# Kernel tuning notes

Hardware: AMD Instinct MI355X
Metric: run time of the kernel (lower is better)

## Reference

```python
import jax, jax.numpy as jnp
import numpy as np

N = 20000          # num nodes
E = 400000         # num edges
F_NODE = 16        # node_features
F_EDGE = 16        # edge_features
H = 128            # hidden_size
D = 16             # node_embedding_dim
DE = 16            # edge_embedding_dim


def setup_inputs() -> dict:
    key = jax.random.key(0)
    ks = jax.random.split(key, 16)
    s = 0.1
    inp = {
        "x": jax.random.normal(ks[0], (N, F_NODE), jnp.float32),
        "edge_index": jax.random.randint(ks[1], (2, E), 0, N, dtype=jnp.int64),
        "edge_attr": jax.random.normal(ks[2], (E, F_EDGE), jnp.float32),
        # node_embedding: Linear(F_NODE, D)
        "Wn": jax.random.normal(ks[3], (F_NODE, D), jnp.float32) * s,
        "bn": jnp.zeros((D,), jnp.float32),
        # edge_embedding: Linear(F_EDGE, DE)
        "We": jax.random.normal(ks[4], (F_EDGE, DE), jnp.float32) * s,
        "be": jnp.zeros((DE,), jnp.float32),
        # shared edge MLP: Linear(F_EDGE, H) -> ReLU -> Linear(H, 2*D*D)
        "W1": jax.random.normal(ks[5], (F_EDGE, H), jnp.float32) * s,
        "b1": jnp.zeros((H,), jnp.float32),
        "W2": jax.random.normal(ks[6], (H, 2 * D * D), jnp.float32) * s,
        "b2": jnp.zeros((2 * D * D,), jnp.float32),
        # per-layer root weights and biases
        "root1": jax.random.normal(ks[7], (D, D), jnp.float32) * s,
        "bias1": jnp.zeros((D,), jnp.float32),
        "root2": jax.random.normal(ks[8], (D, D), jnp.float32) * s,
        "bias2": jnp.zeros((D,), jnp.float32),
    }
    return inp


def _graph_conv(h, src, dst, edge_attr, W1, b1, W2, b2, root, bias):
    # per-edge weight from shared MLP: [E, 2D*D] -> [E, 2D, D]
    w = jnp.maximum(edge_attr @ W1 + b1, 0.0) @ W2 + b2
    w = w.reshape(E, 2 * D, D)
    # gather endpoint features; x_i = target, x_j = source (PyG flow)
    nf = jnp.concatenate([h[dst], h[src]], axis=1)           # [E, 2D]
    msg = jnp.einsum("ek,ekd->ed", nf, w)                    # [E, D]
    aggr = jax.ops.segment_sum(msg, dst, num_segments=N)     # [N, D]
    return aggr + h @ root + bias


def reference(x, edge_index, edge_attr, Wn, bn, We, be, W1, b1, W2, b2,
              root1, bias1, root2, bias2):
    src, dst = edge_index[0], edge_index[1]
    h = jnp.maximum(x @ Wn + bn, 0.0)                        # node embedding [N, D]
    h = _graph_conv(h, src, dst, edge_attr, W1, b1, W2, b2, root1, bias1)
    h = _graph_conv(h, src, dst, edge_attr, W1, b1, W2, b2, root2, bias2)
    ee = jnp.maximum(edge_attr @ We + be, 0.0)               # edge embedding [E, DE]
    return h, edge_index, ee, jax.nn.log_softmax(ee, axis=-1)
```

## Files before the change

kernel.cpp:

```cpp
#include <hip/hip_runtime.h>
#include <hip/hip_bf16.h>


#define NN 20000
#define NE 400000

typedef unsigned short u16;
typedef unsigned int   u32;
typedef __attribute__((ext_vector_type(8))) short short8;
typedef __attribute__((ext_vector_type(4))) float f32x4;

__device__ __forceinline__ float bf2f(u16 h) {
  union { u32 u; float f; } v; v.u = ((u32)h) << 16; return v.f;
}
__device__ __forceinline__ u16 f2bf(float f) {
  union { float f; u32 u; } v; v.f = f;
  return (u16)((v.u + 0x7FFFu + ((v.u >> 16) & 1u)) >> 16);
}
__device__ __forceinline__ float ldf(const void* p, size_t i, int f32m) {
  return f32m ? ((const float*)p)[i] : bf2f(((const u16*)p)[i]);
}
__device__ __forceinline__ int ldi(const void* p, size_t i, int i64m) {
  return i64m ? (int)((const long long*)p)[i] : ((const int*)p)[i];
}
__device__ __forceinline__ void stf(void* p, size_t i, float v, int f32m) {
  if (f32m) ((float*)p)[i] = v; else ((u16*)p)[i] = f2bf(v);
}

__global__ void k_detect(const u16* __restrict__ x16,
                         const int* __restrict__ ei32, int* __restrict__ flags) {
  int t = blockIdx.x * 256 + threadIdx.x;
  int found_f32 = 0, found_hi = 0;
  for (int i = t; i < NN * 16; i += 64 * 256) {
    u16 v = x16[i];
    if ((v & 0x7F80u) == 0x7F80u) found_f32 = 1;
  }
  for (int i = t; i < 200000; i += 64 * 256)
    if (ei32[2 * i + 1] != 0) found_hi = 1;
  if (__any(found_f32) && (threadIdx.x & 63) == 0) atomicOr(&flags[0], 1);
  if (__any(found_hi) && (threadIdx.x & 63) == 0) atomicOr(&flags[1], 1);
}

__global__ void k_pack_w2(const void* __restrict__ W2, u16* __restrict__ w2p,
                          const int* __restrict__ flags) {
  const int f32m = flags[0];
  int t = blockIdx.x * 256 + threadIdx.x;
  if (t >= 32 * 4 * 64) return;
  int lane = t & 63;
  int ks = (t >> 6) & 3;
  int kb = t >> 8;
  int n = lane & 15, q = lane >> 4;
  for (int j = 0; j < 8; ++j) {
    int h = ks * 32 + q * 8 + j;
    w2p[(size_t)t * 8 + j] = f2bf(ldf(W2, (size_t)h * 512 + kb * 16 + n, f32m));
  }
}

__global__ void k_pack_w1(const void* __restrict__ W1, u16* __restrict__ w1p,
                          const int* __restrict__ flags) {
  const int f32m = flags[0];
  int t = blockIdx.x * 256 + threadIdx.x;
  if (t >= 8 * 64) return;
  int lane = t & 63;
  int n = t >> 6;
  int col = n * 16 + (lane & 15), q = lane >> 4;
  for (int j = 0; j < 8; ++j) {
    int kk = q * 8 + j;
    w1p[(size_t)t * 8 + j] = (kk < 16) ? f2bf(ldf(W1, (size_t)kk * 128 + col, f32m)) : (u16)0;
  }
}

__global__ void k_pack_qd(const void* __restrict__ W2, u16* __restrict__ w2q,
                          u16* __restrict__ w2d, const int* __restrict__ flags) {
  const int f32m = flags[0];
  int t = blockIdx.x * 256 + threadIdx.x;
  if (t >= 8192) return;
  int lane = t & 63, q = lane >> 4, l16 = lane & 15;
  if (t < 4096) {
    int kc = t >> 6;
#pragma unroll
    for (int jj = 0; jj < 8; ++jj) {
      int kj = kc * 32 + q * 8 + jj;
      int j = kj >> 4, ks = kj & 15;
      w2q[(size_t)t * 8 + jj] =
          f2bf(ldf(W2, (size_t)j * 512 + (16 + ks) * 16 + l16, f32m));
    }
  } else {
    int u = t - 4096;
    int ct = u >> 8;
    int jc = (u >> 6) & 3;
#pragma unroll
    for (int jj = 0; jj < 8; ++jj) {
      int j = jc * 32 + q * 8 + jj;
      w2d[(size_t)u * 8 + jj] =
          f2bf(ldf(W2, (size_t)j * 512 + ct * 16 + l16, f32m));
    }
  }
}

__global__ void k_embed(const void* __restrict__ x, const void* __restrict__ Wn,
                        const void* __restrict__ bn, float* __restrict__ h0,
                        const int* __restrict__ flags) {
  const int f32m = flags[0];
  int t = blockIdx.x * 256 + threadIdx.x;
  if (t >= NN * 16) return;
  int n = t >> 4, d = t & 15;
  float acc = ldf(bn, d, f32m);
  for (int k = 0; k < 16; ++k)
    acc += ldf(x, n * 16 + k, f32m) * ldf(Wn, k * 16 + d, f32m);
  h0[t] = fmaxf(acc, 0.f);
}

__global__ void k_count(const void* __restrict__ ei, int* __restrict__ cnt,
                        const int* __restrict__ flags) {
  const int i64m = !flags[1];
  int i = blockIdx.x * 256 + threadIdx.x;
  if (i < NE) atomicAdd(&cnt[ldi(ei, NE + i, i64m)], 1);
}

__global__ void k_scan(const int* __restrict__ cnt, int* __restrict__ rowptr,
                       int* __restrict__ cursor) {
  __shared__ int part[1024];
  int t = threadIdx.x;
  int base = t * 20;
  int s = 0;
  for (int j = 0; j < 20; ++j) { int idx = base + j; if (idx < NN) s += cnt[idx]; }
  part[t] = s;
  __syncthreads();
  for (int off = 1; off < 1024; off <<= 1) {
    int v = (t >= off) ? part[t - off] : 0;
    __syncthreads();
    part[t] += v;
    __syncthreads();
  }
  int run = t ? part[t - 1] : 0;
  for (int j = 0; j < 20; ++j) {
    int idx = base + j;
    if (idx < NN) {
      int c = cnt[idx];
      rowptr[idx] = run; cursor[idx] = run; run += c;
    }
  }
  if (t == 1023) rowptr[NN] = part[1023];
}

__global__ void k_scanp(const int* __restrict__ deg, int* __restrict__ prow,
                        int* __restrict__ cursor) {
  __shared__ int part[1024];
  int t = threadIdx.x;
  int base = t * 20;
  int s = 0;
  for (int j = 0; j < 20; ++j) {
    int idx = base + j;
    if (idx < NN) s += (deg[idx] + 31) & ~31;
  }
  part[t] = s;
  __syncthreads();
  for (int off = 1; off < 1024; off <<= 1) {
    int v = (t >= off) ? part[t - off] : 0;
    __syncthreads();
    part[t] += v;
    __syncthreads();
  }
  int run = t ? part[t - 1] : 0;
  for (int j = 0; j < 20; ++j) {
    int idx = base + j;
    if (idx < NN) {
      int p = (deg[idx] + 31) & ~31;
      prow[idx] = run; cursor[idx] = run; run += p;
    }
  }
  if (t == 1023) prow[NN] = part[1023];
}

__global__ void k_scatter(const void* __restrict__ ei, int* __restrict__ cursor,
                          int* __restrict__ inv, int* __restrict__ srcp,
                          const void* __restrict__ ea, u16* __restrict__ eap,
                          const int* __restrict__ flags) {
  const int f32m = flags[0], i64m = !flags[1];
  int i = blockIdx.x * 256 + threadIdx.x;
  if (i >= NE) return;
  int d = ldi(ei, NE + i, i64m);
  int pos = atomicAdd(&cursor[d], 1);
  if (inv)   inv[i] = pos;
  if (srcp)  srcp[pos] = ldi(ei, i, i64m);
  if (eap) {
    union { uint4 q[2]; u16 h[16]; } o;
    if (f32m) {
      const float4* ep = (const float4*)((const float*)ea + (size_t)i * 16);
      float4 a = ep[0], b = ep[1], c = ep[2], e4 = ep[3];
      o.h[0]=f2bf(a.x);  o.h[1]=f2bf(a.y);  o.h[2]=f2bf(a.z);  o.h[3]=f2bf(a.w);
      o.h[4]=f2bf(b.x);  o.h[5]=f2bf(b.y);  o.h[6]=f2bf(b.z);  o.h[7]=f2bf(b.w);
      o.h[8]=f2bf(c.x);  o.h[9]=f2bf(c.y);  o.h[10]=f2bf(c.z); o.h[11]=f2bf(c.w);
      o.h[12]=f2bf(e4.x); o.h[13]=f2bf(e4.y); o.h[14]=f2bf(e4.z); o.h[15]=f2bf(e4.w);
    } else {
      const uint4* ep = (const uint4*)((const u16*)ea + (size_t)i * 16);
      o.q[0] = ep[0]; o.q[1] = ep[1];
    }
    uint4* dp = (uint4*)(eap + (size_t)pos * 16);
    dp[0] = o.q[0]; dp[1] = o.q[1];
  }
}

__launch_bounds__(256)
__attribute__((amdgpu_waves_per_eu(2, 4)))
__global__ void k_node(const int* __restrict__ prow,
                       const int* __restrict__ deg,
                       const int* __restrict__ srcperm,
                       const u16* __restrict__ eap,
                       const float* __restrict__ hin,
                       const u16* __restrict__ w1p,
                       const void* __restrict__ b1,
                       const u16* __restrict__ w2q,
                       const u16* __restrict__ w2d,
                       const void* __restrict__ b2,
                       const void* __restrict__ root,
                       const void* __restrict__ bias,
                       float* __restrict__ hout, void* __restrict__ out,
                       const int* __restrict__ flags) {
  __shared__ u16   T_lds[4 * 2048];
  __shared__ u32   S_lds[4 * 64];
  __shared__ float hs_lds[4 * 16];
  __shared__ float h_lds[4 * 16];
  __shared__ float part_lds[4 * 256];
  __shared__ float b1_lds[128];
  __shared__ u16   w1_lds[4096];
  __shared__ u32   BB_lds[4][320];
  const int f32m = flags[0];
  const int t = threadIdx.x;
  const int lane = t & 63, w = t >> 6;
  const int q = lane >> 4, l16 = lane & 15;
  const int n0 = blockIdx.x * 4;
  const short8 z8 = {0,0,0,0,0,0,0,0};

  if (t < 64) h_lds[t] = hin[(size_t)(n0 + (t >> 4)) * 16 + (t & 15)];
  if (t < 128) b1_lds[t] = ldf(b1, t, f32m);
  {
    const uint4* src = (const uint4*)w1p;
    uint4* dst = (uint4*)w1_lds;
    dst[t] = src[t];
    dst[t + 256] = src[t + 256];
  }

  short8 ONES;
  { union { u32 u[4]; short8 s; } o;
    o.u[0] = 0x3F803F80u; o.u[1] = 0x3F803F80u;
    o.u[2] = 0x3F803F80u; o.u[3] = 0x3F803F80u; ONES = o.s; }

  __syncthreads();

  const int nb = w;
  {
    const int n  = n0 + nb;
    const int beg = prow[n];
    const int end = beg + deg[n];

    f32x4 accT[8];
    float S8[8];
    f32x4 accH = {0.f, 0.f, 0.f, 0.f};
#pragma unroll
    for (int c = 0; c < 8; ++c) {
      accT[c][0] = 0.f; accT[c][1] = 0.f; accT[c][2] = 0.f; accT[c][3] = 0.f;
      S8[c] = 0.f;
    }

    for (int g = beg; g < end; g += 32) {
      int src_l = (lane < 32) ? srcperm[g + lane] : 0;
      union { u32 u[4]; short8 s; } Ahi, Alo, Amk;
#pragma unroll
      for (int jp = 0; jp < 4; ++jp) {
        const int k0 = q * 8 + 2 * jp, k1 = k0 + 1;
        int s0 = __shfl(src_l, k0);
        int s1 = __shfl(src_l, k1);
        float h0 = hin[(size_t)s0 * 16 + l16];
        float h1 = hin[(size_t)s1 * 16 + l16];
        const int v0 = (g + k0 < end);
        const int v1 = (g + k1 < end);
        h0 = v0 ? h0 : 0.f;
        h1 = v1 ? h1 : 0.f;
        union { float f; u32 u; } b0, b1u; b0.f = h0; b1u.f = h1;
        u32 hi0 = b0.u >> 16, hi1 = b1u.u >> 16;
        union { u32 u; float f; } r0, r1; r0.u = hi0 << 16; r1.u = hi1 << 16;
        u32 lo0 = f2bf(h0 - r0.f), lo1 = f2bf(h1 - r1.f);
        Ahi.u[jp] = hi0 | (hi1 << 16);
        Alo.u[jp] = lo0 | (lo1 << 16);
        Amk.u[jp] = (v0 ? 0x3F80u : 0u) | (v1 ? 0x3F800000u : 0u);
      }

      short8 ea0 = z8, ea1 = z8;
      if (q < 2) {
        ea0 = *(const short8*)(eap + (size_t)(g + l16) * 16 + q * 8);
        ea1 = *(const short8*)(eap + (size_t)(g + 16 + l16) * 16 + q * 8);
      }

#pragma unroll
      for (int c = 0; c < 8; ++c) {
        short8 Wf = *(const short8*)&w1_lds[c * 512 + lane * 8];
        f32x4 ca = {0.f, 0.f, 0.f, 0.f}, cb = {0.f, 0.f, 0.f, 0.f};
        ca = __builtin_amdgcn_mfma_f32_16x16x32_bf16(ea0, Wf, ca, 0, 0, 0);
        cb = __builtin_amdgcn_mfma_f32_16x16x32_bf16(ea1, Wf, cb, 0, 0, 0);
        float bb = b1_lds[c * 16 + l16];
        u32 p00 = (u32)f2bf(fmaxf(ca[0] + bb, 0.f)) |
                  ((u32)f2bf(fmaxf(ca[1] + bb, 0.f)) << 16);
        u32 p01 = (u32)f2bf(fmaxf(ca[2] + bb, 0.f)) |
                  ((u32)f2bf(fmaxf(ca[3] + bb, 0.f)) << 16);
        u32 p10 = (u32)f2bf(fmaxf(cb[0] + bb, 0.f)) |
                  ((u32)f2bf(fmaxf(cb[1] + bb, 0.f)) << 16);
        u32 p11 = (u32)f2bf(fmaxf(cb[2] + bb, 0.f)) |
                  ((u32)f2bf(fmaxf(cb[3] + bb, 0.f)) << 16);
        u32* bw = &BB_lds[w][l16 * 20];
        uint2 w0; w0.x = p00; w0.y = p01;
        uint2 w1v; w1v.x = p10; w1v.y = p11;
        *(uint2*)&bw[q * 2]     = w0;
        *(uint2*)&bw[8 + q * 2] = w1v;
        short8 Bf = *(const short8*)&bw[q * 4];
        accT[c] = __builtin_amdgcn_mfma_f32_16x16x32_bf16(Ahi.s, Bf, accT[c], 0, 0, 0);
        accT[c] = __builtin_amdgcn_mfma_f32_16x16x32_bf16(Alo.s, Bf, accT[c], 0, 0, 0);
        f32x4 cs = {0.f, 0.f, 0.f, 0.f};
        cs = __builtin_amdgcn_mfma_f32_16x16x32_bf16(Amk.s, Bf, cs, 0, 0, 0);
        S8[c] += cs[0];
      }
      accH = __builtin_amdgcn_mfma_f32_16x16x32_bf16(Ahi.s, ONES, accH, 0, 0, 0);
      accH = __builtin_amdgcn_mfma_f32_16x16x32_bf16(Alo.s, ONES, accH, 0, 0, 0);
    }

    {
      char* Tl = (char*)T_lds;
#pragma unroll
      for (int c = 0; c < 8; ++c) {
        u32 p0 = (u32)f2bf(accT[c][0]) | ((u32)f2bf(accT[c][1]) << 16);
        u32 p1 = (u32)f2bf(accT[c][2]) | ((u32)f2bf(accT[c][3]) << 16);
        int b   = (c * 16 + l16) * 32 + q * 8;
        int key = ((nb ^ (c * 8 + (l16 >> 1))) & 7) << 4;
        uint2 pv; pv.x = p0; pv.y = p1;
        *(uint2*)(Tl + (size_t)nb * 4096 + (b ^ key)) = pv;
      }
      if (q == 0) {
        u16* s16 = (u16*)S_lds;
#pragma unroll
        for (int c = 0; c < 8; ++c)
          s16[nb * 128 + c * 16 + l16] = f2bf(S8[c]);
      }
      if (l16 == 0) *(f32x4*)&hs_lds[nb * 16 + q * 4] = accH;
    }
  }
  __syncthreads();

  const int row = l16;
  f32x4 c1 = {0.f, 0.f, 0.f, 0.f};
  {
    const short8* w2qf = (const short8*)w2q;
#pragma unroll
    for (int kk = 0; kk < 16; ++kk) {
      int kc = w * 16 + kk;
      int off = ((row & 3) * 4096 + kc * 64 + q * 16) ^ ((((row ^ kc) & 7)) << 4);
      short8 af = *(const short8*)((const char*)T_lds + off);
      if (row >= 4) af = z8;
      short8 bf = w2qf[kc * 64 + lane];
      c1 = __builtin_amdgcn_mfma_f32_16x16x32_bf16(af, bf, c1, 0, 0, 0);
    }
  }
  f32x4 c2_0 = {0,0,0,0}, c2_1 = {0,0,0,0}, c2_2 = {0,0,0,0}, c2_3 = {0,0,0,0};
  {
    short8 as0, as1, as2, as3;
    {
      const u32* sb = S_lds + (row & 3) * 64 + q * 4;
      as0 = *(const short8*)(sb + 0);
      as1 = *(const short8*)(sb + 16);
      as2 = *(const short8*)(sb + 32);
      as3 = *(const short8*)(sb + 48);
      if (row >= 4) { as0 = z8; as1 = z8; as2 = z8; as3 = z8; }
    }
    const short8* w2df = (const short8*)w2d;
#pragma unroll
    for (int ci = 0; ci < 4; ++ci) {
      int ct = w * 4 + ci;
      f32x4 cc = {0.f, 0.f, 0.f, 0.f};
      cc = __builtin_amdgcn_mfma_f32_16x16x32_bf16(as0, w2df[(ct * 4 + 0) * 64 + lane], cc, 0, 0, 0);
      cc = __builtin_amdgcn_mfma_f32_16x16x32_bf16(as1, w2df[(ct * 4 + 1) * 64 + lane], cc, 0, 0, 0);
      cc = __builtin_amdgcn_mfma_f32_16x16x32_bf16(as2, w2df[(ct * 4 + 2) * 64 + lane], cc, 0, 0, 0);
      cc = __builtin_amdgcn_mfma_f32_16x16x32_bf16(as3, w2df[(ct * 4 + 3) * 64 + lane], cc, 0, 0, 0);
      if (ci == 0) c2_0 = cc; else if (ci == 1) c2_1 = cc;
      else if (ci == 2) c2_2 = cc; else c2_3 = cc;
    }
  }
#pragma unroll
  for (int r = 0; r < 4; ++r) {
    int nrow = q * 4 + r;
    const float* hp = h_lds + (nrow & 3) * 16 + w * 4;
    float a = c1[r];
    a += hp[0] * c2_0[r];
    a += hp[1] * c2_1[r];
    a += hp[2] * c2_2[r];
    a += hp[3] * c2_3[r];
    part_lds[w * 256 + nrow * 16 + l16] = a;
  }
  __syncthreads();

  if (t < 64) {
    int nb2 = t >> 4, d = t & 15;
    int n = n0 + nb2;
    float acc = part_lds[nb2 * 16 + d] + part_lds[256 + nb2 * 16 + d] +
                part_lds[512 + nb2 * 16 + d] + part_lds[768 + nb2 * 16 + d];
    float dg = (float)deg[n];
    acc += ldf(bias, d, f32m);
#pragma unroll
    for (int k = 0; k < 16; ++k) {
      float hv = h_lds[nb2 * 16 + k];
      acc += hv * (ldf(root, (size_t)k * 16 + d, f32m) +
                   dg * ldf(b2, (size_t)k * 16 + d, f32m));
      acc += hs_lds[nb2 * 16 + k] * ldf(b2, (size_t)256 + k * 16 + d, f32m);
    }
    if (hout) hout[(size_t)n * 16 + d] = acc;
    else      stf(out, (size_t)n * 16 + d, acc, f32m);
  }
}

__launch_bounds__(256, 2)
__global__ void k_edge(const void* __restrict__ ea, const void* __restrict__ ei,
                       const float* __restrict__ hprev,
                       const u16* __restrict__ w2p, const u16* __restrict__ w1p,
                       const void* __restrict__ b1, const void* __restrict__ b2,
                       u16* __restrict__ msg16, float* __restrict__ aggr,
                       const int* __restrict__ inv,
                       const int* __restrict__ flags, int use_csr) {
  __shared__ u16   a2_lds[128 * 136];
  __shared__ float nfT[32 * 132];
  __shared__ float msg_lds[128 * 17];
  __shared__ float b1_lds[128];
  __shared__ int   dst_lds[128];

  const int f32m = flags[0], i64m = !flags[1];
  const int t = threadIdx.x;
  const int lane = t & 63, w = t >> 6;
  const int q = lane >> 4, l16 = lane & 15;
  const int e0 = blockIdx.x * 128;

  short8 B[8][4];
  {
    const short8* w2pf = (const short8*)w2p;
#pragma unroll
    for (int i = 0; i < 8; ++i)
#pragma unroll
      for (int ks = 0; ks < 4; ++ks)
        B[i][ks] = w2pf[((w * 8 + i) * 4 + ks) * 64 + lane];
  }
  float b2v[8];
#pragma unroll
  for (int i = 0; i < 8; ++i) b2v[i] = ldf(b2, (w * 8 + i) * 16 + l16, f32m);
  short8 W1f[8];
  {
    const short8* w1pf = (const short8*)w1p;
#pragma unroll
    for (int n = 0; n < 8; ++n) W1f[n] = w1pf[n * 64 + lane];
  }
  if (t < 128) b1_lds[t] = ldf(b1, t, f32m);

  {
    int e = t >> 1, hh = t & 1;
    int node = hh ? ldi(ei, e0 + e, i64m) : ldi(ei, NE + e0 + e, i64m);
    const float4* hp = (const float4*)(hprev + (size_t)node * 16);
    float4 h0v = hp[0], h1v = hp[1], h2v = hp[2], h3v = hp[3];
    float* col = nfT + (size_t)(hh * 16) * 132 + e;
    col[0 * 132] = h0v.x; col[1 * 132] = h0v.y; col[2 * 132] = h0v.z; col[3 * 132] = h0v.w;
    col[4 * 132] = h1v.x; col[5 * 132] = h1v.y; col[6 * 132] = h1v.z; col[7 * 132] = h1v.w;
    col[8 * 132] = h2v.x; col[9 * 132] = h2v.y; col[10 * 132] = h2v.z; col[11 * 132] = h2v.w;
    col[12 * 132] = h3v.x; col[13 * 132] = h3v.y; col[14 * 132] = h3v.z; col[15 * 132] = h3v.w;
    if (!hh) {
      if (use_csr) dst_lds[e] = inv[e0 + e];
      else         dst_lds[e] = node;
    }
    float* mz = msg_lds + e * 17 + hh * 8;
#pragma unroll
    for (int k2 = 0; k2 < 8; ++k2) mz[k2] = 0.f;
  }
  __syncthreads();

#pragma unroll
  for (int mm = 0; mm < 2; ++mm) {
    int m = w * 2 + mm;
    union { short8 s; u16 h[8]; } ua;
    if (q < 2) {
      if (f32m) {
        const float* er = (const float*)ea + ((size_t)(e0 + m * 16 + l16) * 16 + q * 8);
        float4 f0 = *(const float4*)er;
        float4 f1 = *(const float4*)(er + 4);
        ua.h[0] = f2bf(f0.x); ua.h[1] = f2bf(f0.y); ua.h[2] = f2bf(f0.z); ua.h[3] = f2bf(f0.w);
        ua.h[4] = f2bf(f1.x); ua.h[5] = f2bf(f1.y); ua.h[6] = f2bf(f1.z); ua.h[7] = f2bf(f1.w);
      } else {
        ua.s = *(const short8*)((const u16*)ea + ((size_t)(e0 + m * 16 + l16) * 16 + q * 8));
      }
    } else {
#pragma unroll
      for (int j = 0; j < 8; ++j) ua.h[j] = 0;
    }
    short8 A = ua.s;
#pragma unroll
    for (int n = 0; n < 8; ++n) {
      f32x4 c = {0.f, 0.f, 0.f, 0.f};
      c = __builtin_amdgcn_mfma_f32_16x16x32_bf16(A, W1f[n], c, 0, 0, 0);
      float bb = b1_lds[n * 16 + l16];
#pragma unroll
      for (int r = 0; r < 4; ++r)
        a2_lds[(m * 16 + q * 4 + r) * 136 + n * 16 + l16] =
            f2bf(fmaxf(c[r] + bb, 0.f));
    }
  }
  __syncthreads();

#pragma unroll 1
  for (int mi = 0; mi < 8; ++mi) {
    int m = (mi + w * 2) & 7;
    const short8* ap = (const short8*)&a2_lds[(m * 16 + l16) * 136 + q * 8];
    short8 A0 = ap[0], A1 = ap[4], A2f = ap[8], A3 = ap[12];
    float mr0 = 0.f, mr1 = 0.f, mr2 = 0.f, mr3 = 0.f;
#pragma unroll
    for (int i = 0; i < 8; ++i) {
      f32x4 c = {b2v[i], b2v[i], b2v[i], b2v[i]};
      c = __builtin_amdgcn_mfma_f32_16x16x32_bf16(A0, B[i][0], c, 0, 0, 0);
      c = __builtin_amdgcn_mfma_f32_16x16x32_bf16(A1, B[i][1], c, 0, 0, 0);
      c = __builtin_amdgcn_mfma_f32_16x16x32_bf16(A2f, B[i][2], c, 0, 0, 0);
      c = __builtin_amdgcn_mfma_f32_16x16x32_bf16(A3, B[i][3], c, 0, 0, 0);
      int kb = w * 8 + i;
      f32x4 nf4 = *(const f32x4*)&nfT[(size_t)kb * 132 + m * 16 + q * 4];
      mr0 += nf4[0] * c[0];
      mr1 += nf4[1] * c[1];
      mr2 += nf4[2] * c[2];
      mr3 += nf4[3] * c[3];
    }
    int eb = (m * 16 + q * 4) * 17 + l16;
    atomicAdd(&msg_lds[eb + 0 * 17], mr0);
    atomicAdd(&msg_lds[eb + 1 * 17], mr1);
    atomicAdd(&msg_lds[eb + 2 * 17], mr2);
    atomicAdd(&msg_lds[eb + 3 * 17], mr3);
  }
  __syncthreads();

  {
    int e = t >> 1, dh = t & 1;
    const float* mp = msg_lds + e * 17 + dh * 8;
    if (use_csr) {
      int pos = dst_lds[e];
      union { uint4 qv; u16 h[8]; } pk;
#pragma unroll
      for (int dd = 0; dd < 8; ++dd) pk.h[dd] = f2bf(mp[dd]);
      *(uint4*)(msg16 + (size_t)pos * 16 + dh * 8) = pk.qv;
    } else {
      int dnode = dst_lds[e];
      float* ap2 = aggr + (size_t)dnode * 16 + dh * 8;
#pragma unroll
      for (int dd = 0; dd < 8; ++dd) atomicAdd(ap2 + dd, mp[dd]);
    }
  }
}

__global__ void k_gather(const u16* __restrict__ msg16,
                         const int* __restrict__ rowptr,
                         const float* __restrict__ h_old,
                         const void* __restrict__ root,
                         const void* __restrict__ bias,
                         float* __restrict__ h_new, void* __restrict__ out,
                         const int* __restrict__ flags) {
  const int f32m = flags[0];
  __shared__ float R[256];
  __shared__ float Bv[16];
  int tt = threadIdx.x;
  R[tt] = ldf(root, tt, f32m);
  if (tt < 16) Bv[tt] = ldf(bias, tt, f32m);
  __syncthreads();
  int t = blockIdx.x * 256 + tt;
  if (t >= NN * 16) return;
  int n = t >> 4, d = t & 15;
  float acc = Bv[d];
#pragma unroll
  for (int k = 0; k < 16; ++k) acc += h_old[n * 16 + k] * R[k * 16 + d];
  int beg = rowptr[n], end = rowptr[n + 1];
  for (int i = beg; i < end; ++i)
    acc += bf2f(msg16[(size_t)i * 16 + d]);
  if (h_new) h_new[t] = acc;
  else       stf(out, t, acc, f32m);
}

__global__ void k_combine(const float* __restrict__ h_old,
                          const float* __restrict__ aggr,
                          const void* __restrict__ root,
                          const void* __restrict__ bias,
                          float* __restrict__ h_new, void* __restrict__ out,
                          const int* __restrict__ flags) {
  const int f32m = flags[0];
  int t = blockIdx.x * 256 + threadIdx.x;
  if (t >= NN * 16) return;
  int n = t >> 4, d = t & 15;
  float acc = aggr[t] + ldf(bias, d, f32m);
  for (int k = 0; k < 16; ++k)
    acc += h_old[n * 16 + k] * ldf(root, (size_t)k * 16 + d, f32m);
  if (h_new) h_new[t] = acc;
  else       stf(out, t, acc, f32m);
}

__global__ void k_ee(const void* __restrict__ ea, const void* __restrict__ We,
                     const void* __restrict__ be, void* __restrict__ out,
                     const int* __restrict__ flags) {
  const int f32m = flags[0];
  __shared__ float W[256];
  __shared__ float Bv[16];
  int t = threadIdx.x;
  W[t] = ldf(We, t, f32m);
  if (t < 16) Bv[t] = ldf(be, t, f32m);
  __syncthreads();
  int e = blockIdx.x * 256 + t;
  if (e >= NE) return;
  float v[16];
  if (f32m) {
    const float4* ep = (const float4*)((const float*)ea + (size_t)e * 16);
    float4 r0 = ep[0], r1 = ep[1], r2 = ep[2], r3 = ep[3];
    v[0]=r0.x; v[1]=r0.y; v[2]=r0.z; v[3]=r0.w;
    v[4]=r1.x; v[5]=r1.y; v[6]=r1.z; v[7]=r1.w;
    v[8]=r2.x; v[9]=r2.y; v[10]=r2.z; v[11]=r2.w;
    v[12]=r3.x; v[13]=r3.y; v[14]=r3.z; v[15]=r3.w;
  } else {
    union { uint4 qv[2]; u16 h[16]; } rw;
    const uint4* ep = (const uint4*)((const u16*)ea + (size_t)e * 16);
    rw.qv[0] = ep[0]; rw.qv[1] = ep[1];
#pragma unroll
    for (int k = 0; k < 16; ++k) v[k] = bf2f(rw.h[k]);
  }
  float o[16];
  float mx = 0.f;
#pragma unroll
  for (int d = 0; d < 16; ++d) {
    float acc = Bv[d];
#pragma unroll
    for (int k = 0; k < 16; ++k) acc += v[k] * W[k * 16 + d];
    acc = fmaxf(acc, 0.f);
    o[d] = acc;
    mx = fmaxf(mx, acc);
  }
  float s = 0.f;
#pragma unroll
  for (int d = 0; d < 16; ++d) s += __expf(o[d] - mx);
  float lse = mx + __logf(s);
  const size_t off_ee = 1120000, off_ls = 7520000;
  if (f32m) {
    union { float4 fv; float f[4]; } pe, pl;
    float* oe = (float*)out + off_ee + (size_t)e * 16;
    float* ol = (float*)out + off_ls + (size_t)e * 16;
#pragma unroll
    for (int g = 0; g < 4; ++g) {
#pragma unroll
      for (int d = 0; d < 4; ++d) { pe.f[d] = o[g*4+d]; pl.f[d] = o[g*4+d] - lse; }
      ((float4*)oe)[g] = pe.fv;
      ((float4*)ol)[g] = pl.fv;
    }
  } else {
    union { uint4 qv[2]; u16 h[16]; } pe, pl;
#pragma unroll
    for (int d = 0; d < 16; ++d) {
      pe.h[d] = f2bf(o[d]);
      pl.h[d] = f2bf(o[d] - lse);
    }
    uint4* oe = (uint4*)((u16*)out + off_ee + (size_t)e * 16);
    uint4* ol = (uint4*)((u16*)out + off_ls + (size_t)e * 16);
    oe[0] = pe.qv[0]; oe[1] = pe.qv[1];
    ol[0] = pl.qv[0]; ol[1] = pl.qv[1];
  }
}

__global__ void k_idx(const void* __restrict__ ei, void* __restrict__ out,
                      const int* __restrict__ flags) {
  const int f32m = flags[0], i64m = !flags[1];
  int i = blockIdx.x * 256 + threadIdx.x;
  if (i >= 2 * NE) return;
  float v = i64m ? (float)((const long long*)ei)[i] : (float)((const int*)ei)[i];
  stf(out, (size_t)320000 + i, v, f32m);
}

extern "C" void kernel_launch(void* const* d_in, const int* in_sizes, int n_in,
                              void* d_out, int out_size, void* d_ws, size_t ws_size,
                              hipStream_t stream) {
  const void* x     = d_in[0];
  const void* ei    = d_in[1];
  const void* ea    = d_in[2];
  const void* Wn    = d_in[3];
  const void* bn    = d_in[4];
  const void* We    = d_in[5];
  const void* be    = d_in[6];
  const void* W1    = d_in[7];
  const void* b1    = d_in[8];
  const void* W2    = d_in[9];
  const void* b2    = d_in[10];
  const void* root1 = d_in[11];
  const void* bias1 = d_in[12];
  const void* root2 = d_in[13];
  const void* bias2 = d_in[14];

  char* ws = (char*)d_ws;
  const size_t need_new = 39659296;

  if (ws_size >= need_new) {
    int*   flags   = (int*)ws;
    float* h0      = (float*)(ws + 16);
    float* h1      = (float*)(ws + 1280016);
    u16*   w1p     = (u16*)(ws + 2560016);
    u16*   w2q     = (u16*)(ws + 2568208);
    u16*   w2d     = (u16*)(ws + 2633744);
    int*   deg     = (int*)(ws + 2699280);
    int*   prow    = (int*)(ws + 2779280);
    int*   cursor  = (int*)(ws + 2859296);
    int*   srcperm = (int*)(ws + 2939296);
    u16*   eap     = (u16*)(ws + 7019296);

    hipMemsetAsync(flags, 0, 16, stream);
    hipMemsetAsync(deg, 0, 80000, stream);
    hipMemsetAsync(srcperm, 0, 36720000, stream);
    k_detect<<<64, 256, 0, stream>>>((const u16*)x, (const int*)ei, flags);
    k_pack_w1<<<2, 256, 0, stream>>>(W1, w1p, flags);
    k_pack_qd<<<32, 256, 0, stream>>>(W2, w2q, w2d, flags);
    k_embed<<<1250, 256, 0, stream>>>(x, Wn, bn, h0, flags);

    k_count<<<1563, 256, 0, stream>>>(ei, deg, flags);
    k_scanp<<<1, 1024, 0, stream>>>(deg, prow, cursor);
    k_scatter<<<1563, 256, 0, stream>>>(ei, cursor, nullptr, srcperm, ea, eap, flags);

    k_node<<<5000, 256, 0, stream>>>(prow, deg, srcperm, eap, h0, w1p, b1, w2q, w2d,
                                     b2, root1, bias1, h1, nullptr, flags);
    k_node<<<5000, 256, 0, stream>>>(prow, deg, srcperm, eap, h1, w1p, b1, w2q, w2d,
                                     b2, root2, bias2, nullptr, d_out, flags);

    k_ee<<<1563, 256, 0, stream>>>(ea, We, be, d_out, flags);
    k_idx<<<3125, 256, 0, stream>>>(ei, d_out, flags);
    return;
  }

  int*   flags  = (int*)ws;
  float* h0     = (float*)(ws + 16);
  float* h1     = (float*)(ws + 1280016);
  u16*   w2p    = (u16*)(ws + 2560016);
  u16*   w1p    = (u16*)(ws + 2691088);
  u16*   msg16  = (u16*)(ws + 2699280);
  int*   rowptr = (int*)(ws + 15499280);
  int*   cursor = (int*)(ws + 15579296);
  int*   inv    = (int*)(ws + 15659296);
  const size_t need_csr = 17259296;
  float* aggr = (float*)(ws + 2699280);
  const int use_csr = (ws_size >= need_csr) ? 1 : 0;

  hipMemsetAsync(flags, 0, 16, stream);
  k_detect<<<64, 256, 0, stream>>>((const u16*)x, (const int*)ei, flags);
  k_pack_w2<<<32, 256, 0, stream>>>(W2, w2p, flags);
  k_pack_w1<<<2, 256, 0, stream>>>(W1, w1p, flags);
  k_embed<<<1250, 256, 0, stream>>>(x, Wn, bn, h0, flags);

  if (use_csr) {
    hipMemsetAsync(cursor, 0, NN * 4, stream);
    k_count<<<1563, 256, 0, stream>>>(ei, cursor, flags);
    k_scan<<<1, 1024, 0, stream>>>(cursor, rowptr, cursor);
    k_scatter<<<1563, 256, 0, stream>>>(ei, cursor, inv, nullptr, nullptr, nullptr, flags);

    k_edge<<<3125, 256, 0, stream>>>(ea, ei, h0, w2p, w1p, b1, b2, msg16, nullptr, inv, flags, 1);
    k_gather<<<1250, 256, 0, stream>>>(msg16, rowptr, h0, root1, bias1, h1, nullptr, flags);
    k_edge<<<3125, 256, 0, stream>>>(ea, ei, h1, w2p, w1p, b1, b2, msg16, nullptr, inv, flags, 1);
    k_gather<<<1250, 256, 0, stream>>>(msg16, rowptr, h1, root2, bias2, nullptr, d_out, flags);
  } else {
    hipMemsetAsync(aggr, 0, (size_t)NN * 16 * 4, stream);
    k_edge<<<3125, 256, 0, stream>>>(ea, ei, h0, w2p, w1p, b1, b2, nullptr, aggr, nullptr, flags, 0);
    k_combine<<<1250, 256, 0, stream>>>(h0, aggr, root1, bias1, h1, nullptr, flags);
    hipMemsetAsync(aggr, 0, (size_t)NN * 16 * 4, stream);
    k_edge<<<3125, 256, 0, stream>>>(ea, ei, h1, w2p, w1p, b1, b2, nullptr, aggr, nullptr, flags, 0);
    k_combine<<<1250, 256, 0, stream>>>(h1, aggr, root2, bias2, nullptr, d_out, flags);
  }

  k_ee<<<1563, 256, 0, stream>>>(ea, We, be, d_out, flags);
  k_idx<<<3125, 256, 0, stream>>>(ei, d_out, flags);
}
```

Measured before the change: 370.0 us.

## Fuse setup kernels into one launch and precompute bf16 hi/lo node features

Merges weight packing, node embedding, degree counting, edge embedding/log-softmax and index output into a single multi-role kernel, cutting several launches and memsets. Node features are also stored as a precomputed bf16 hi/lo pair, so the gather loop in k_node no longer does the split per edge. The MLP bias is folded into the MFMA accumulator init, and k_detect now uses more blocks. This costs extra workspace and an extra store per node feature.

```diff
diff --git a/kernel.cpp b/kernel.cpp
--- a/kernel.cpp
+++ b/kernel.cpp
@@ -17,6 +17,12 @@
   union { float f; u32 u; } v; v.f = f;
   return (u16)((v.u + 0x7FFFu + ((v.u >> 16) & 1u)) >> 16);
 }
+__device__ __forceinline__ u32 splitpk(float h) {
+  union { float f; u32 u; } uu; uu.f = h;
+  u32 hi = uu.u >> 16;
+  union { u32 u; float f; } rr; rr.u = hi << 16;
+  return (hi << 16) | (u32)f2bf(h - rr.f);
+}
 __device__ __forceinline__ float ldf(const void* p, size_t i, int f32m) {
   return f32m ? ((const float*)p)[i] : bf2f(((const u16*)p)[i]);
 }
@@ -30,15 +36,147 @@
 __global__ void k_detect(const u16* __restrict__ x16,
                          const int* __restrict__ ei32, int* __restrict__ flags) {
   int t = blockIdx.x * 256 + threadIdx.x;
+  int stride = gridDim.x * 256;
   int found_f32 = 0, found_hi = 0;
-  for (int i = t; i < NN * 16; i += 64 * 256) {
+  for (int i = t; i < NN * 16; i += stride) {
     u16 v = x16[i];
     if ((v & 0x7F80u) == 0x7F80u) found_f32 = 1;
   }
-  for (int i = t; i < 200000; i += 64 * 256)
+  for (int i = t; i < 200000; i += stride)
     if (ei32[2 * i + 1] != 0) found_hi = 1;
   if (__any(found_f32) && (threadIdx.x & 63) == 0) atomicOr(&flags[0], 1);
   if (__any(found_hi) && (threadIdx.x & 63) == 0) atomicOr(&flags[1], 1);
+}
+
+__global__ void k_misc(const void* __restrict__ W1, u16* __restrict__ w1p,
+                       const void* __restrict__ W2, u16* __restrict__ w2q,
+                       u16* __restrict__ w2d,
+                       const void* __restrict__ x, const void* __restrict__ Wn,
+                       const void* __restrict__ bn, float* __restrict__ h0,
+                       u32* __restrict__ h0s,
+                       const void* __restrict__ ei, int* __restrict__ deg,
+                       const void* __restrict__ ea, const void* __restrict__ We,
+                       const void* __restrict__ be, void* __restrict__ out,
+                       const int* __restrict__ flags) {
+  const int f32m = flags[0], i64m = !flags[1];
+  const int b = blockIdx.x, tid = threadIdx.x;
+  __shared__ float W[256];
+  __shared__ float Bv[16];
+
+  if (b < 2) {
+    int t = b * 256 + tid;
+    int lane = t & 63;
+    int n = t >> 6;
+    int col = n * 16 + (lane & 15), q = lane >> 4;
+    for (int j = 0; j < 8; ++j) {
+      int kk = q * 8 + j;
+      w1p[(size_t)t * 8 + j] = (kk < 16) ? f2bf(ldf(W1, (size_t)kk * 128 + col, f32m)) : (u16)0;
+    }
+  } else if (b < 34) {
+    int t = (b - 2) * 256 + tid;
+    int lane = t & 63, q = lane >> 4, l16 = lane & 15;
+    if (t < 4096) {
+      int kc = t >> 6;
+#pragma unroll
+      for (int jj = 0; jj < 8; ++jj) {
+        int kj = kc * 32 + q * 8 + jj;
+        int j = kj >> 4, ks = kj & 15;
+        w2q[(size_t)t * 8 + jj] =
+            f2bf(ldf(W2, (size_t)j * 512 + (16 + ks) * 16 + l16, f32m));
+      }
+    } else {
+      int u = t - 4096;
+      int ct = u >> 8;
+      int jc = (u >> 6) & 3;
+#pragma unroll
+      for (int jj = 0; jj < 8; ++jj) {
+        int j = jc * 32 + q * 8 + jj;
+        w2d[(size_t)u * 8 + jj] =
+            f2bf(ldf(W2, (size_t)j * 512 + ct * 16 + l16, f32m));
+      }
+    }
+  } else if (b < 1284) {
+    int t = (b - 34) * 256 + tid;
+    if (t < NN * 16) {
+      int n = t >> 4, d = t & 15;
+      float acc = ldf(bn, d, f32m);
+      for (int k = 0; k < 16; ++k)
+        acc += ldf(x, n * 16 + k, f32m) * ldf(Wn, k * 16 + d, f32m);
+      float h = fmaxf(acc, 0.f);
+      h0[t] = h;
+      h0s[t] = splitpk(h);
+    }
+  } else if (b < 2847) {
+    int i = (b - 1284) * 256 + tid;
+    if (i < NE) atomicAdd(&deg[ldi(ei, NE + i, i64m)], 1);
+  } else if (b < 4410) {
+    int t = tid;
+    W[t] = ldf(We, t, f32m);
+    if (t < 16) Bv[t] = ldf(be, t, f32m);
+    __syncthreads();
+    int e = (b - 2847) * 256 + t;
+    if (e >= NE) return;
+    float v[16];
+    if (f32m) {
+      const float4* ep = (const float4*)((const float*)ea + (size_t)e * 16);
+      float4 r0 = ep[0], r1 = ep[1], r2 = ep[2], r3 = ep[3];
+      v[0]=r0.x; v[1]=r0.y; v[2]=r0.z; v[3]=r0.w;
+      v[4]=r1.x; v[5]=r1.y; v[6]=r1.z; v[7]=r1.w;
+      v[8]=r2.x; v[9]=r2.y; v[10]=r2.z; v[11]=r2.w;
+      v[12]=r3.x; v[13]=r3.y; v[14]=r3.z; v[15]=r3.w;
+    } else {
+      union { uint4 qv[2]; u16 h[16]; } rw;
+      const uint4* ep = (const uint4*)((const u16*)ea + (size_t)e * 16);
+      rw.qv[0] = ep[0]; rw.qv[1] = ep[1];
+#pragma unroll
+      for (int k = 0; k < 16; ++k) v[k] = bf2f(rw.h[k]);
+    }
+    float o[16];
+    float mx = 0.f;
+#pragma unroll
+    for (int d = 0; d < 16; ++d) {
+      float acc = Bv[d];
+#pragma unroll
+      for (int k = 0; k < 16; ++k) acc += v[k] * W[k * 16 + d];
+      acc = fmaxf(acc, 0.f);
+      o[d] = acc;
+      mx = fmaxf(mx, acc);
+    }
+    float s = 0.f;
+#pragma unroll
+    for (int d = 0; d < 16; ++d) s += __expf(o[d] - mx);
+    float lse = mx + __logf(s);
+    const size_t off_ee = 1120000, off_ls = 7520000;
+    if (f32m) {
+      union { float4 fv; float f[4]; } pe, pl;
+      float* oe = (float*)out + off_ee + (size_t)e * 16;
+      float* ol = (float*)out + off_ls + (size_t)e * 16;
+#pragma unroll
+      for (int g = 0; g < 4; ++g) {
+#pragma unroll
+        for (int d = 0; d < 4; ++d) { pe.f[d] = o[g*4+d]; pl.f[d] = o[g*4+d] - lse; }
+        ((float4*)oe)[g] = pe.fv;
+        ((float4*)ol)[g] = pl.fv;
+      }
+    } else {
+      union { uint4 qv[2]; u16 h[16]; } pe, pl;
+#pragma unroll
+      for (int d = 0; d < 16; ++d) {
+        pe.h[d] = f2bf(o[d]);
+        pl.h[d] = f2bf(o[d] - lse);
+      }
+      uint4* oe = (uint4*)((u16*)out + off_ee + (size_t)e * 16);
+      uint4* ol = (uint4*)((u16*)out + off_ls + (size_t)e * 16);
+      oe[0] = pe.qv[0]; oe[1] = pe.qv[1];
+      ol[0] = pl.qv[0]; ol[1] = pl.qv[1];
+    }
+  } else {
+    int i = (b - 4410) * 256 + tid;
+    if (i < 2 * NE) {
+      float v = i64m ? (float)((const long long*)ei)[i] : (float)((const int*)ei)[i];
+      stf(out, (size_t)320000 + i, v, f32m);
+    }
+  }
 }
 
 __global__ void k_pack_w2(const void* __restrict__ W2, u16* __restrict__ w2p,
@@ -67,34 +205,6 @@
   for (int j = 0; j < 8; ++j) {
     int kk = q * 8 + j;
     w1p[(size_t)t * 8 + j] = (kk < 16) ? f2bf(ldf(W1, (size_t)kk * 128 + col, f32m)) : (u16)0;
-  }
-}
-
-__global__ void k_pack_qd(const void* __restrict__ W2, u16* __restrict__ w2q,
-                          u16* __restrict__ w2d, const int* __restrict__ flags) {
-  const int f32m = flags[0];
-  int t = blockIdx.x * 256 + threadIdx.x;
-  if (t >= 8192) return;
-  int lane = t & 63, q = lane >> 4, l16 = lane & 15;
-  if (t < 4096) {
-    int kc = t >> 6;
-#pragma unroll
-    for (int jj = 0; jj < 8; ++jj) {
-      int kj = kc * 32 + q * 8 + jj;
-      int j = kj >> 4, ks = kj & 15;
-      w2q[(size_t)t * 8 + jj] =
-          f2bf(ldf(W2, (size_t)j * 512 + (16 + ks) * 16 + l16, f32m));
-    }
-  } else {
-    int u = t - 4096;
-    int ct = u >> 8;
-    int jc = (u >> 6) & 3;
-#pragma unroll
-    for (int jj = 0; jj < 8; ++jj) {
-      int j = jc * 32 + q * 8 + jj;
-      w2d[(size_t)u * 8 + jj] =
-          f2bf(ldf(W2, (size_t)j * 512 + ct * 16 + l16, f32m));
-    }
   }
 }
 
@@ -209,6 +319,7 @@
                        const int* __restrict__ srcperm,
                        const u16* __restrict__ eap,
                        const float* __restrict__ hin,
+                       const u32* __restrict__ hsin,
                        const u16* __restrict__ w1p,
                        const void* __restrict__ b1,
                        const u16* __restrict__ w2q,
@@ -216,7 +327,8 @@
                        const void* __restrict__ b2,
                        const void* __restrict__ root,
                        const void* __restrict__ bias,
-                       float* __restrict__ hout, void* __restrict__ out,
+                       float* __restrict__ hout, u32* __restrict__ hsout,
+                       void* __restrict__ out,
                        const int* __restrict__ flags) {
   __shared__ u16   T_lds[4 * 2048];
   __shared__ u32   S_lds[4 * 64];
@@ -272,18 +384,14 @@
         const int k0 = q * 8 + 2 * jp, k1 = k0 + 1;
         int s0 = __shfl(src_l, k0);
         int s1 = __shfl(src_l, k1);
-        float h0 = hin[(size_t)s0 * 16 + l16];
-        float h1 = hin[(size_t)s1 * 16 + l16];
+        u32 v0d = hsin[(size_t)s0 * 16 + l16];
+        u32 v1d = hsin[(size_t)s1 * 16 + l16];
         const int v0 = (g + k0 < end);
         const int v1 = (g + k1 < end);
-        h0 = v0 ? h0 : 0.f;
-        h1 = v1 ? h1 : 0.f;
-        union { float f; u32 u; } b0, b1u; b0.f = h0; b1u.f = h1;
-        u32 hi0 = b0.u >> 16, hi1 = b1u.u >> 16;
-        union { u32 u; float f; } r0, r1; r0.u = hi0 << 16; r1.u = hi1 << 16;
-        u32 lo0 = f2bf(h0 - r0.f), lo1 = f2bf(h1 - r1.f);
-        Ahi.u[jp] = hi0 | (hi1 << 16);
-        Alo.u[jp] = lo0 | (lo1 << 16);
+        if (!v0) v0d = 0;
+        if (!v1) v1d = 0;
+        Ahi.u[jp] = (v0d >> 16) | (v1d & 0xFFFF0000u);
+        Alo.u[jp] = (v0d & 0xFFFFu) | (v1d << 16);
         Amk.u[jp] = (v0 ? 0x3F80u : 0u) | (v1 ? 0x3F800000u : 0u);
       }
 
@@ -296,18 +404,18 @@
 #pragma unroll
       for (int c = 0; c < 8; ++c) {
         short8 Wf = *(const short8*)&w1_lds[c * 512 + lane * 8];
-        f32x4 ca = {0.f, 0.f, 0.f, 0.f}, cb = {0.f, 0.f, 0.f, 0.f};
+        float bb = b1_lds[c * 16 + l16];
+        f32x4 ca = {bb, bb, bb, bb}, cb = {bb, bb, bb, bb};
         ca = __builtin_amdgcn_mfma_f32_16x16x32_bf16(ea0, Wf, ca, 0, 0, 0);
         cb = __builtin_amdgcn_mfma_f32_16x16x32_bf16(ea1, Wf, cb, 0, 0, 0);
-        float bb = b1_lds[c * 16 + l16];
-        u32 p00 = (u32)f2bf(fmaxf(ca[0] + bb, 0.f)) |
-                  ((u32)f2bf(fmaxf(ca[1] + bb, 0.f)) << 16);
-        u32 p01 = (u32)f2bf(fmaxf(ca[2] + bb, 0.f)) |
-                  ((u32)f2bf(fmaxf(ca[3] + bb, 0.f)) << 16);
-        u32 p10 = (u32)f2bf(fmaxf(cb[0] + bb, 0.f)) |
-                  ((u32)f2bf(fmaxf(cb[1] + bb, 0.f)) << 16);
-        u32 p11 = (u32)f2bf(fmaxf(cb[2] + bb, 0.f)) |
-                  ((u32)f2bf(fmaxf(cb[3] + bb, 0.f)) << 16);
+        u32 p00 = (u32)f2bf(fmaxf(ca[0], 0.f)) |
+                  ((u32)f2bf(fmaxf(ca[1], 0.f)) << 16);
+        u32 p01 = (u32)f2bf(fmaxf(ca[2], 0.f)) |
+                  ((u32)f2bf(fmaxf(ca[3], 0.f)) << 16);
+        u32 p10 = (u32)f2bf(fmaxf(cb[0], 0.f)) |
+                  ((u32)f2bf(fmaxf(cb[1], 0.f)) << 16);
+        u32 p11 = (u32)f2bf(fmaxf(cb[2], 0.f)) |
+                  ((u32)f2bf(fmaxf(cb[3], 0.f)) << 16);
         u32* bw = &BB_lds[w][l16 * 20];
         uint2 w0; w0.x = p00; w0.y = p01;
         uint2 w1v; w1v.x = p10; w1v.y = p11;
@@ -411,8 +519,12 @@
                    dg * ldf(b2, (size_t)k * 16 + d, f32m));
       acc += hs_lds[nb2 * 16 + k] * ldf(b2, (size_t)256 + k * 16 + d, f32m);
     }
-    if (hout) hout[(size_t)n * 16 + d] = acc;
-    else      stf(out, (size_t)n * 16 + d, acc, f32m);
+    if (hout) {
+      hout[(size_t)n * 16 + d] = acc;
+      hsout[(size_t)n * 16 + d] = splitpk(acc);
+    } else {
+      stf(out, (size_t)n * 16 + d, acc, f32m);
+    }
   }
 }
 
@@ -695,40 +807,35 @@
   const void* bias2 = d_in[14];
 
   char* ws = (char*)d_ws;
-  const size_t need_new = 39659296;
+  const size_t need_new = 42219296;
 
   if (ws_size >= need_new) {
     int*   flags   = (int*)ws;
-    float* h0      = (float*)(ws + 16);
-    float* h1      = (float*)(ws + 1280016);
-    u16*   w1p     = (u16*)(ws + 2560016);
-    u16*   w2q     = (u16*)(ws + 2568208);
-    u16*   w2d     = (u16*)(ws + 2633744);
-    int*   deg     = (int*)(ws + 2699280);
-    int*   prow    = (int*)(ws + 2779280);
-    int*   cursor  = (int*)(ws + 2859296);
-    int*   srcperm = (int*)(ws + 2939296);
-    u16*   eap     = (u16*)(ws + 7019296);
-
-    hipMemsetAsync(flags, 0, 16, stream);
-    hipMemsetAsync(deg, 0, 80000, stream);
+    int*   deg     = (int*)(ws + 16);
+    float* h0      = (float*)(ws + 80016);
+    u32*   h0s     = (u32*)(ws + 1360016);
+    float* h1      = (float*)(ws + 2640016);
+    u32*   h1s     = (u32*)(ws + 3920016);
+    u16*   w1p     = (u16*)(ws + 5200016);
+    u16*   w2q     = (u16*)(ws + 5208208);
+    u16*   w2d     = (u16*)(ws + 5273744);
+    int*   prow    = (int*)(ws + 5339280);
+    int*   cursor  = (int*)(ws + 5419296);
+    int*   srcperm = (int*)(ws + 5499296);
+    u16*   eap     = (u16*)(ws + 9579296);
+
+    hipMemsetAsync(ws, 0, 80016, stream);
     hipMemsetAsync(srcperm, 0, 36720000, stream);
-    k_detect<<<64, 256, 0, stream>>>((const u16*)x, (const int*)ei, flags);
-    k_pack_w1<<<2, 256, 0, stream>>>(W1, w1p, flags);
-    k_pack_qd<<<32, 256, 0, stream>>>(W2, w2q, w2d, flags);
-    k_embed<<<1250, 256, 0, stream>>>(x, Wn, bn, h0, flags);
-
-    k_count<<<1563, 256, 0, stream>>>(ei, deg, flags);
+    k_detect<<<128, 256, 0, stream>>>((const u16*)x, (const int*)ei, flags);
+    k_misc<<<7535, 256, 0, stream>>>(W1, w1p, W2, w2q, w2d, x, Wn, bn, h0, h0s,
+                                     ei, deg, ea, We, be, d_out, flags);
     k_scanp<<<1, 1024, 0, stream>>>(deg, prow, cursor);
     k_scatter<<<1563, 256, 0, stream>>>(ei, cursor, nullptr, srcperm, ea, eap, flags);
 
-    k_node<<<5000, 256, 0, stream>>>(prow, deg, srcperm, eap, h0, w1p, b1, w2q, w2d,
-                                     b2, root1, bias1, h1, nullptr, flags);
-    k_node<<<5000, 256, 0, stream>>>(prow, deg, srcperm, eap, h1, w1p, b1, w2q, w2d,
-                                     b2, root2, bias2, nullptr, d_out, flags);
-
-    k_ee<<<1563, 256, 0, stream>>>(ea, We, be, d_out, flags);
-    k_idx<<<3125, 256, 0, stream>>>(ei, d_out, flags);
+    k_node<<<5000, 256, 0, stream>>>(prow, deg, srcperm, eap, h0, h0s, w1p, b1,
+                                     w2q, w2d, b2, root1, bias1, h1, h1s, nullptr, flags);
+    k_node<<<5000, 256, 0, stream>>>(prow, deg, srcperm, eap, h1, h1s, w1p, b1,
+                                     w2q, w2d, b2, root2, bias2, nullptr, nullptr, d_out, flags);
     return;
   }
 
```

New measurement: 383.0 us. +3.5%, slower.
